# Optimization experiments

Hardware: AMD Instinct MI355X
Metric: run time of the kernel (lower is better)

The kernel has to match this reference:

```python
import jax, jax.numpy as jnp
import numpy as np
from jax import lax

BS, T, GRID, FEAT = 64, 32, 36, 256
HID, PROJ, NCLS = 256, 128, 6
MLP_IN = FEAT + HID  # 512


def _lstm(h, c, xs, Wih, Whh, bih, bhh):
    # xs: (L, bs, in); PyTorch gate order i, f, g, o
    def step(carry, x):
        h, c = carry
        g = x @ Wih.T + bih + h @ Whh.T + bhh
        i_, f_, g_, o_ = jnp.split(g, 4, axis=-1)
        c = jax.nn.sigmoid(f_) * c + jax.nn.sigmoid(i_) * jnp.tanh(g_)
        h = jax.nn.sigmoid(o_) * jnp.tanh(c)
        return (h, c), None
    (h, c), _ = lax.scan(step, (h, c), xs)
    return h, c


def setup_inputs() -> dict:
    key = jax.random.key(0)
    ks = iter(jax.random.split(key, 32))
    r = lambda *s: jax.random.normal(next(ks), s, dtype=jnp.float32) * 0.05
    inp = {
        'cnn_feat_seq': jax.random.normal(next(ks), (BS, T, GRID, FEAT), dtype=jnp.float32),
        'gaze_seq': jax.random.normal(next(ks), (BS, T, 3), dtype=jnp.float32),
        # spatial attention layer
        'W_lh': r(PROJ, HID), 'b_lh': r(PROJ),      # linear_lstm
        'W_cn': r(PROJ, FEAT), 'b_cn': r(PROJ),     # linear_cnn
        'w_wt': r(1, PROJ),                         # linear_weight (no bias)
        # gaze LSTM
        'Wih': r(4 * HID, 3), 'Whh': r(4 * HID, HID), 'bih': r(4 * HID), 'bhh': r(4 * HID),
        # init hidden / cell MLPs (Linear, Tanh, Linear, Tanh)
        'Wh1': r(HID, 3), 'bh1': r(HID), 'Wh2': r(HID, HID), 'bh2': r(HID),
        'Wc1': r(HID, 3), 'bc1': r(HID), 'Wc2': r(HID, HID), 'bc2': r(HID),
        # mlp classifier (3 linears, no activations)
        'Wm1': r(MLP_IN, MLP_IN), 'bm1': r(MLP_IN),
        'Wm2': r(MLP_IN, MLP_IN), 'bm2': r(MLP_IN),
        'Wm3': r(NCLS, MLP_IN), 'bm3': r(NCLS),
    }
    return inp


def reference(cnn_feat_seq, gaze_seq, W_lh, b_lh, W_cn, b_cn, w_wt,
              Wih, Whh, bih, bhh, Wh1, bh1, Wh2, bh2, Wc1, bc1, Wc2, bc2,
              Wm1, bm1, Wm2, bm2, Wm3, bm3):
    bs, num_frame, grid, feat = cnn_feat_seq.shape
    # init LSTM state: Sequential(Linear,Tanh,Linear,Tanh) then an extra F.tanh
    mg = jnp.mean(gaze_seq, axis=1)  # (bs, 3)
    h = jnp.tanh(jnp.tanh(jnp.tanh(mg @ Wh1.T + bh1) @ Wh2.T + bh2))
    c = jnp.tanh(jnp.tanh(jnp.tanh(mg @ Wc1.T + bc1) @ Wc2.T + bc2))

    preds = []
    for i in range(num_frame):
        V = cnn_feat_seq[:, i]  # (bs, grid, feat)
        # attention scores; same Linear applied per grid cell -> compute once
        Hl = h @ W_lh.T + b_lh                       # (bs, proj)
        Vp = V @ W_cn.T + b_cn                       # (bs, grid, proj)
        z = jnp.tanh(Hl[:, None, :] + Vp) @ w_wt[0]  # (bs, grid)
        # replicate torch.cat(dim=0).view(bs, grid): flat order is grid-major
        z_scrambled = z.T.reshape(bs, grid)
        sw = jax.nn.softmax(z_scrambled, axis=1)     # (bs, grid)
        spatial_feat = jnp.einsum('bgf,bg->bf', V, sw)
        # LSTM over growing gaze prefix (frame 0: first step only)
        L = 1 if i == 0 else i
        xs = jnp.transpose(gaze_seq[:, :L, :], (1, 0, 2))  # (L, bs, 3)
        h, c = _lstm(h, c, xs, Wih, Whh, bih, bhh)
        fc = jnp.concatenate([spatial_feat, h], axis=1)    # (bs, 512)
        pred = ((fc @ Wm1.T + bm1) @ Wm2.T + bm2) @ Wm3.T + bm3
        preds.append(pred[None])  # (1, bs, ncls)
    # torch.cat(pred_all, 1) over (1,bs,ncls) pieces -> (1, T*bs, ncls)
    return jnp.concatenate(preds, axis=1)
```

## Files before the change

### kernel.cpp

```cpp
#include <hip/hip_runtime.h>
#include <math.h>


typedef _Float16 h2_t __attribute__((ext_vector_type(2)));

#if __has_builtin(__builtin_amdgcn_fdot2)
#define HAVE_FDOT2 1
#else
#define HAVE_FDOT2 0
#endif

__device__ __forceinline__ float dot2(unsigned w, unsigned h, float acc) {
#if HAVE_FDOT2
  return __builtin_amdgcn_fdot2(__builtin_bit_cast(h2_t, w),
                                __builtin_bit_cast(h2_t, h), acc, false);
#else
  h2_t a = __builtin_bit_cast(h2_t, w);
  h2_t b = __builtin_bit_cast(h2_t, h);
  return acc + (float)a[0] * (float)b[0] + (float)a[1] * (float)b[1];
#endif
}

__device__ __forceinline__ unsigned pack2(float a, float b) {
  h2_t p;
  p[0] = (_Float16)a;
  p[1] = (_Float16)b;
  return __builtin_bit_cast(unsigned, p);
}

__device__ __forceinline__ float sigmoid_f(float x) {
  return __builtin_amdgcn_rcpf(1.f + __expf(-x));
}
__device__ __forceinline__ float tanh_f(float x) {
  return 1.f - 2.f * __builtin_amdgcn_rcpf(1.f + __expf(2.f * x));
}

__global__ void k_pack_lstm(const float* __restrict__ Whh,
                            unsigned* __restrict__ wlds_pack,
                            unsigned* __restrict__ wst) {
  const int idx = blockIdx.x * 256 + threadIdx.x;
  if (idx < 32768) {
    const int row = idx >> 5, pair = idx & 31;
    wlds_pack[idx] =
        pack2(Whh[row * 256 + 2 * pair], Whh[row * 256 + 2 * pair + 1]);
  } else {
    const int rel = idx - 32768;
    const int m = rel >> 12, row = (rel >> 2) & 1023, d = rel & 3;
    const int pair = 32 + 4 * m + d;
    wst[rel] = pack2(Whh[row * 256 + 2 * pair], Whh[row * 256 + 2 * pair + 1]);
  }
}

__global__ void k_packh2(const float* __restrict__ src,
                         unsigned* __restrict__ dst, int n) {
  const int i = blockIdx.x * 256 + threadIdx.x;
  if (i < n) dst[i] = pack2(src[2 * i], src[2 * i + 1]);
}

__global__ void k_xg(const float* __restrict__ gaze,
                     const float* __restrict__ Wih,
                     const float* __restrict__ bih,
                     const float* __restrict__ bhh,
                     float* __restrict__ xg) {
  const int idx = blockIdx.x * 256 + threadIdx.x;
  if (idx >= 31 * 64 * 1024) return;
  const int j = idx & 1023;
  const int b = (idx >> 10) & 63;
  const int t = idx >> 16;
  const float* gz = gaze + (b * 32 + t) * 3;
  xg[idx] = gz[0] * Wih[j * 3 + 0] + gz[1] * Wih[j * 3 + 1] +
            gz[2] * Wih[j * 3 + 2] + bih[j] + bhh[j];
}

__global__ void k_init(const float* __restrict__ gaze,
                       const float* __restrict__ Wh1, const float* __restrict__ bh1,
                       const float* __restrict__ Wh2, const float* __restrict__ bh2,
                       const float* __restrict__ Wc1, const float* __restrict__ bc1,
                       const float* __restrict__ Wc2, const float* __restrict__ bc2,
                       float* __restrict__ HH, float* __restrict__ c0) {
  const int b = blockIdx.x;
  const int tid = threadIdx.x;
  __shared__ float mg[3];
  __shared__ float t1h[256], t1c[256];
  if (tid < 3) {
    float s = 0.f;
    for (int t = 0; t < 32; t++) s += gaze[(b * 32 + t) * 3 + tid];
    mg[tid] = s * (1.f / 32.f);
  }
  __syncthreads();
  {
    float a = mg[0] * Wh1[tid * 3 + 0] + mg[1] * Wh1[tid * 3 + 1] +
              mg[2] * Wh1[tid * 3 + 2] + bh1[tid];
    t1h[tid] = tanhf(a);
    float c = mg[0] * Wc1[tid * 3 + 0] + mg[1] * Wc1[tid * 3 + 1] +
              mg[2] * Wc1[tid * 3 + 2] + bc1[tid];
    t1c[tid] = tanhf(c);
  }
  __syncthreads();
  float s1 = bh2[tid], s2 = bc2[tid];
  for (int k = 0; k < 256; k++) {
    s1 += t1h[k] * Wh2[tid * 256 + k];
    s2 += t1c[k] * Wc2[tid * 256 + k];
  }
  HH[b * 256 + tid] = tanhf(tanhf(s1));
  c0[b * 256 + tid] = tanhf(tanhf(s2));
}

__global__ __launch_bounds__(1024) void k_fused(
    const float* __restrict__ xg, const unsigned* __restrict__ wst,
    const unsigned* __restrict__ wlds_pack, const float* __restrict__ c0,
    float* __restrict__ HH, const float* __restrict__ cnn,
    const unsigned* __restrict__ wcn_h2, const float* __restrict__ bcn,
    unsigned* __restrict__ Vp, int nvp, const float* __restrict__ Wm1,
    unsigned* __restrict__ wm1d, const float* __restrict__ Wm2,
    unsigned* __restrict__ wm2d, const float* __restrict__ Wm3,
    unsigned* __restrict__ wm3d, const float* __restrict__ Wlh,
    unsigned* __restrict__ wlhd) {
  const int bid = blockIdx.x;
  const int tid = threadIdx.x;
  __shared__ __align__(16) unsigned smem[38016];

  if (bid < 64) {
    const int b = bid;
    unsigned* wlds = smem;
    float* actl = (float*)(smem + 36864);
    unsigned* h2l = smem + 36864 + 1024;

    for (int i = tid; i < 1024 * 32; i += 1024) {
      const int row = i >> 5, p = i & 31;
      wlds[row * 36 + p] = wlds_pack[i];
    }

    float cst = (tid < 256) ? c0[b * 256 + tid] : 0.f;
    if (tid < 256) ((_Float16*)h2l)[tid] = (_Float16)HH[b * 256 + tid];
    __syncthreads();

    const unsigned* wA = &wlds[tid * 36];
    const uint4* wstp = (const uint4*)wst + tid;
    const bool is_g = (tid >= 512) & (tid < 768);
    float hval = 0.f;

    for (int frame = 0; frame < 32; frame++) {
      const int L = frame ? frame : 1;
      for (int t = 0; t < L; t++) {
        const float xgv = xg[(t * 64 + b) * 1024 + tid];
        float ga0 = 0.f, ga1 = 0.f;
#pragma unroll
        for (int q = 0; q < 8; q++) {
          const uint4 h4 = *(const uint4*)&h2l[4 * q];
          const uint4 a4 = *(const uint4*)&wA[4 * q];
          if ((q & 1) == 0) {
            ga0 = dot2(a4.x, h4.x, ga0);
            ga0 = dot2(a4.y, h4.y, ga0);
            ga0 = dot2(a4.z, h4.z, ga0);
            ga0 = dot2(a4.w, h4.w, ga0);
          } else {
            ga1 = dot2(a4.x, h4.x, ga1);
            ga1 = dot2(a4.y, h4.y, ga1);
            ga1 = dot2(a4.z, h4.z, ga1);
            ga1 = dot2(a4.w, h4.w, ga1);
          }
        }
#pragma unroll
        for (int m = 0; m < 24; m++) {
          const uint4 wq = wstp[m << 10];
          const uint4 h4 = *(const uint4*)&h2l[32 + 4 * m];
          if ((m & 1) == 0) {
            ga0 = dot2(wq.x, h4.x, ga0);
            ga0 = dot2(wq.y, h4.y, ga0);
            ga0 = dot2(wq.z, h4.z, ga0);
            ga0 = dot2(wq.w, h4.w, ga0);
          } else {
            ga1 = dot2(wq.x, h4.x, ga1);
            ga1 = dot2(wq.y, h4.y, ga1);
            ga1 = dot2(wq.z, h4.z, ga1);
            ga1 = dot2(wq.w, h4.w, ga1);
          }
        }
        const float g = ga0 + ga1 + xgv;
        const float act = is_g ? tanh_f(g) : sigmoid_f(g);
        actl[tid] = act;
        __syncthreads();
        if (tid < 256) {
          const float i_ = actl[tid];
          const float f_ = actl[256 + tid];
          const float g_ = actl[512 + tid];
          const float o_ = actl[768 + tid];
          cst = f_ * cst + i_ * g_;
          hval = o_ * tanh_f(cst);
          ((_Float16*)h2l)[tid] = (_Float16)hval;
        }
        __syncthreads();
      }
      if (tid < 256) HH[((frame + 1) * 64 + b) * 256 + tid] = hval;
    }
  } else if (bid < 64 + nvp) {
    const int vb = bid - 64;
    const int i = vb / 18, rt = vb - 18 * i;
    const int r0 = rt * 128;
    unsigned* As = smem;
    unsigned* Bs = smem + 16896;
    float* bcs = (float*)(smem + 33792);

    for (int idx = tid; idx < 128 * 128; idx += 1024) {
      const int r = idx >> 7, kp = idx & 127;
      const int R = r0 + r;
      const int b = R / 36, g = R - b * 36;
      const float* src = cnn + (((size_t)b * 32 + i) * 36 + g) * 256 + 2 * kp;
      As[r * 132 + kp] = pack2(src[0], src[1]);
    }
    for (int idx = tid; idx < 128 * 128; idx += 1024) {
      const int o = idx >> 7, kp = idx & 127;
      Bs[o * 132 + kp] = wcn_h2[o * 128 + kp];
    }
    if (tid < 128) bcs[tid] = bcn[tid];
    __syncthreads();

    const int ry = tid >> 4, px = tid & 15;
    float acc[2][8];
#pragma unroll
    for (int k = 0; k < 2; k++)
#pragma unroll
      for (int m = 0; m < 8; m++)
        acc[k][m] = bcs[32 * (m >> 1) + 2 * px + (m & 1)];
    for (int kb = 0; kb < 32; kb++) {
      uint4 a4[2], b4[8];
#pragma unroll
      for (int k = 0; k < 2; k++)
        a4[k] = *(const uint4*)&As[(64 * k + ry) * 132 + 4 * kb];
#pragma unroll
      for (int m = 0; m < 8; m++)
        b4[m] = *(const uint4*)&Bs[(32 * (m >> 1) + 2 * px + (m & 1)) * 132 + 4 * kb];
#pragma unroll
      for (int k = 0; k < 2; k++)
#pragma unroll
        for (int m = 0; m < 8; m++) {
          acc[k][m] = dot2(a4[k].x, b4[m].x, acc[k][m]);
          acc[k][m] = dot2(a4[k].y, b4[m].y, acc[k][m]);
          acc[k][m] = dot2(a4[k].z, b4[m].z, acc[k][m]);
          acc[k][m] = dot2(a4[k].w, b4[m].w, acc[k][m]);
        }
    }
#pragma unroll
    for (int k = 0; k < 2; k++) {
      const int R = r0 + 64 * k + ry;
#pragma unroll
      for (int jj = 0; jj < 4; jj++)
        Vp[((size_t)i * 2304 + R) * 64 + 16 * jj + px] =
            pack2(acc[k][2 * jj], acc[k][2 * jj + 1]);
    }
  } else {
    const int pb = bid - 64 - nvp;
    if (pb < 8) {
      const int base = pb * 16384;
      for (int j = tid; j < 16384; j += 1024)
        wm1d[base + j] = pack2(Wm1[2 * (base + j)], Wm1[2 * (base + j) + 1]);
    } else if (pb < 16) {
      const int base = (pb - 8) * 16384;
      for (int j = tid; j < 16384; j += 1024)
        wm2d[base + j] = pack2(Wm2[2 * (base + j)], Wm2[2 * (base + j) + 1]);
    } else {
      for (int j = tid; j < 1536; j += 1024)
        wm3d[j] = pack2(Wm3[2 * j], Wm3[2 * j + 1]);
      for (int j = tid; j < 16384; j += 1024)
        wlhd[j] = pack2(Wlh[2 * j], Wlh[2 * j + 1]);
    }
  }
}

__global__ void k_zfin(const unsigned* __restrict__ Vp,
                       const float* __restrict__ Hl,
                       const float* __restrict__ wwt,
                       float* __restrict__ zbuf) {
  const int bid = blockIdx.x;
  const int i = bid / 18, rt = bid - 18 * i;
  const int r0 = rt * 128;
  const int tid = threadIdx.x;
  __shared__ float Hls[5 * 128];
  __shared__ float wws[128];
  __shared__ float zpart[128 * 16];
  const int bmin = r0 / 36;
  for (int idx = tid; idx < 5 * 128; idx += 256) {
    const int bb = bmin + (idx >> 7);
    if (bb < 64) Hls[idx] = Hl[(i * 64 + bb) * 128 + (idx & 127)];
  }
  if (tid < 128) wws[tid] = wwt[tid];
  __syncthreads();
  const int ry = tid >> 4, px = tid & 15;
#pragma unroll
  for (int k = 0; k < 8; k++) {
    const int r = 16 * k + ry;
    const int R = r0 + r;
    const int b = R / 36;
    const unsigned* vr = Vp + ((size_t)i * 2304 + R) * 64;
    const float* Hr = &Hls[(b - bmin) * 128];
    float z = 0.f;
#pragma unroll
    for (int jj = 0; jj < 4; jj++) {
      const int pp = 16 * jj + px;
      const h2_t pr = __builtin_bit_cast(h2_t, vr[pp]);
      z += wws[2 * pp] * tanh_f(Hr[2 * pp] + (float)pr[0]);
      z += wws[2 * pp + 1] * tanh_f(Hr[2 * pp + 1] + (float)pr[1]);
    }
    zpart[r * 16 + px] = z;
  }
  __syncthreads();
  if (tid < 128) {
    float z = 0.f;
#pragma unroll
    for (int x = 0; x < 16; x++) z += zpart[tid * 16 + x];
    const int R = r0 + tid;
    const int b = R / 36, g = R - b * 36;
    zbuf[(i * 64 + b) * 36 + g] = z;
  }
}

__global__ void k_hl(const float* __restrict__ HH,
                     const unsigned* __restrict__ wlh_h2,
                     const float* __restrict__ blh, float* __restrict__ Hl) {
  const int i = blockIdx.x;
  const int tid = threadIdx.x;
  __shared__ __align__(16) unsigned Ah[64 * 132];
  __shared__ __align__(16) unsigned Bh[128 * 132];
  for (int idx = tid; idx < 64 * 128; idx += 256) {
    const int r = idx >> 7, kp = idx & 127;
    const float* s = HH + ((size_t)(i * 64 + r)) * 256 + 2 * kp;
    Ah[r * 132 + kp] = pack2(s[0], s[1]);
  }
  for (int idx = tid; idx < 128 * 128; idx += 256) {
    const int o = idx >> 7, kp = idx & 127;
    Bh[o * 132 + kp] = wlh_h2[o * 128 + kp];
  }
  __syncthreads();
  const int ry = tid >> 4, px = tid & 15;
  float acc[4][8];
#pragma unroll
  for (int k = 0; k < 4; k++)
#pragma unroll
    for (int j = 0; j < 8; j++) acc[k][j] = 0.f;
  for (int kb = 0; kb < 32; kb++) {
    uint4 a4[4], b4[8];
#pragma unroll
    for (int k = 0; k < 4; k++) a4[k] = *(const uint4*)&Ah[(16 * k + ry) * 132 + 4 * kb];
#pragma unroll
    for (int j = 0; j < 8; j++) b4[j] = *(const uint4*)&Bh[(16 * j + px) * 132 + 4 * kb];
#pragma unroll
    for (int k = 0; k < 4; k++)
#pragma unroll
      for (int j = 0; j < 8; j++) {
        acc[k][j] = dot2(a4[k].x, b4[j].x, acc[k][j]);
        acc[k][j] = dot2(a4[k].y, b4[j].y, acc[k][j]);
        acc[k][j] = dot2(a4[k].z, b4[j].z, acc[k][j]);
        acc[k][j] = dot2(a4[k].w, b4[j].w, acc[k][j]);
      }
  }
#pragma unroll
  for (int k = 0; k < 4; k++)
#pragma unroll
    for (int j = 0; j < 8; j++)
      Hl[(i * 64 + 16 * k + ry) * 128 + 16 * j + px] = acc[k][j] + blh[16 * j + px];
}

__global__ void k_att_z(const float* __restrict__ cnn,
                        const unsigned* __restrict__ wcn_h2,
                        const float* __restrict__ bcn,
                        const float* __restrict__ Hl,
                        const float* __restrict__ wwt,
                        float* __restrict__ zbuf) {
  const int bid = blockIdx.x;
  const int i = bid / 18, rt = bid - 18 * i;
  const int tid = threadIdx.x;
  const int r0 = rt * 128;
  __shared__ __align__(16) unsigned As[128 * 132];
  __shared__ __align__(16) unsigned Bs[128 * 132];
  __shared__ float zpart[128 * 16];
  __shared__ float Hls[5 * 128];
  __shared__ float wws[128];
  __shared__ float bcs[128];

  for (int idx = tid; idx < 128 * 128; idx += 256) {
    const int r = idx >> 7, kp = idx & 127;
    const int R = r0 + r;
    const int b = R / 36, g = R - b * 36;
    const float* src = cnn + (((size_t)b * 32 + i) * 36 + g) * 256 + 2 * kp;
    As[r * 132 + kp] = pack2(src[0], src[1]);
  }
  for (int idx = tid; idx < 128 * 128; idx += 256) {
    const int o = idx >> 7, kp = idx & 127;
    Bs[o * 132 + kp] = wcn_h2[o * 128 + kp];
  }
  const int bmin = r0 / 36;
  for (int idx = tid; idx < 5 * 128; idx += 256) {
    const int bb = bmin + (idx >> 7);
    if (bb < 64) Hls[idx] = Hl[(i * 64 + bb) * 128 + (idx & 127)];
  }
  if (tid < 128) {
    wws[tid] = wwt[tid];
    bcs[tid] = bcn[tid];
  }
  __syncthreads();

  const int ry = tid >> 4, px = tid & 15;
  float acc[8][8];
#pragma unroll
  for (int k = 0; k < 8; k++)
#pragma unroll
    for (int j = 0; j < 8; j++) acc[k][j] = bcs[16 * j + px];
  for (int kb = 0; kb < 32; kb++) {
    uint4 a4[8], b4[8];
#pragma unroll
    for (int k = 0; k < 8; k++) a4[k] = *(const uint4*)&As[(16 * k + ry) * 132 + 4 * kb];
#pragma unroll
    for (int j = 0; j < 8; j++) b4[j] = *(const uint4*)&Bs[(16 * j + px) * 132 + 4 * kb];
#pragma unroll
    for (int k = 0; k < 8; k++)
#pragma unroll
      for (int j = 0; j < 8; j++) {
        acc[k][j] = dot2(a4[k].x, b4[j].x, acc[k][j]);
        acc[k][j] = dot2(a4[k].y, b4[j].y, acc[k][j]);
        acc[k][j] = dot2(a4[k].z, b4[j].z, acc[k][j]);
        acc[k][j] = dot2(a4[k].w, b4[j].w, acc[k][j]);
      }
  }
#pragma unroll
  for (int k = 0; k < 8; k++) {
    const int r = 16 * k + ry;
    const int R = r0 + r;
    const int b = R / 36;
    const float* HlRow = &Hls[(b - bmin) * 128];
    float zp = 0.f;
#pragma unroll
    for (int j = 0; j < 8; j++) {
      const int po = 16 * j + px;
      zp += wws[po] * tanh_f(HlRow[po] + acc[k][j]);
    }
    zpart[r * 16 + px] = zp;
  }
  __syncthreads();
  if (tid < 128) {
    float z = 0.f;
#pragma unroll
    for (int x = 0; x < 16; x++) z += zpart[tid * 16 + x];
    const int R = r0 + tid;
    const int b = R / 36, g = R - b * 36;
    zbuf[(i * 64 + b) * 36 + g] = z;
  }
}

__global__ void k_att_sf(const float* __restrict__ cnn,
                         const float* __restrict__ zbuf,
                         const float* __restrict__ HH,
                         float* __restrict__ fc) {
  const int bid = blockIdx.x;
  const int i = bid >> 6, b = bid & 63;
  const int tid = threadIdx.x;
  __shared__ float zl[36];
  __shared__ float el[40];
  __shared__ float red[1];
  if (tid < 36) {
    const int idx = b * 36 + tid;
    zl[tid] = zbuf[(i * 64 + (idx & 63)) * 36 + (idx >> 6)];
  }
  __syncthreads();
  if (tid == 0) {
    float m = zl[0];
    for (int g = 1; g < 36; g++) m = fmaxf(m, zl[g]);
    float s = 0.f;
    for (int g = 0; g < 36; g++) {
      const float e = __expf(zl[g] - m);
      el[g] = e;
      s += e;
    }
    red[0] = 1.f / s;
  }
  __syncthreads();
  const float inv = red[0];
  float accv = 0.f;
  const float* Vb = cnn + (((size_t)b * 32 + i) * 36) * 256 + tid;
#pragma unroll 4
  for (int g = 0; g < 36; g++) accv += el[g] * Vb[g * 256];
  fc[(size_t)bid * 512 + tid] = accv * inv;
  fc[(size_t)bid * 512 + 256 + tid] = HH[((i + 1) * 64 + b) * 256 + tid];
}

template <int SRCMODE>
__global__ void k_mlp(const void* __restrict__ src,
                      const unsigned* __restrict__ wh2,
                      const float* __restrict__ bias,
                      unsigned* __restrict__ dst) {
  const int bid = blockIdx.x;
  const int nb = bid >> 2, ob = bid & 3;
  const int n0 = nb * 64, o0 = ob * 128;
  const int tid = threadIdx.x;
  __shared__ __align__(16) unsigned As[64 * 132];
  __shared__ __align__(16) unsigned Bs[128 * 132];
  const int ry = tid >> 4, px = tid & 15;
  float acc[4][8];
#pragma unroll
  for (int k = 0; k < 4; k++)
#pragma unroll
    for (int m = 0; m < 8; m++)
      acc[k][m] = bias[o0 + 32 * (m >> 1) + 2 * px + (m & 1)];
  for (int kc = 0; kc < 2; kc++) {
    __syncthreads();
    for (int idx = tid; idx < 64 * 128; idx += 256) {
      const int r = idx >> 7, kp = idx & 127;
      if (SRCMODE == 0) {
        const float* s = (const float*)src + ((size_t)(n0 + r)) * 512 + kc * 256 + 2 * kp;
        As[r * 132 + kp] = pack2(s[0], s[1]);
      } else {
        As[r * 132 + kp] = ((const unsigned*)src)[((size_t)(n0 + r)) * 256 + kc * 128 + kp];
      }
    }
    for (int idx = tid; idx < 128 * 128; idx += 256) {
      const int o = idx >> 7, kp = idx & 127;
      Bs[o * 132 + kp] = wh2[((size_t)(o0 + o)) * 256 + kc * 128 + kp];
    }
    __syncthreads();
    for (int kb = 0; kb < 32; kb++) {
      uint4 a4[4], b4[8];
#pragma unroll
      for (int k = 0; k < 4; k++)
        a4[k] = *(const uint4*)&As[(16 * k + ry) * 132 + 4 * kb];
#pragma unroll
      for (int m = 0; m < 8; m++)
        b4[m] = *(const uint4*)&Bs[(32 * (m >> 1) + 2 * px + (m & 1)) * 132 + 4 * kb];
#pragma unroll
      for (int k = 0; k < 4; k++)
#pragma unroll
        for (int m = 0; m < 8; m++) {
          acc[k][m] = dot2(a4[k].x, b4[m].x, acc[k][m]);
          acc[k][m] = dot2(a4[k].y, b4[m].y, acc[k][m]);
          acc[k][m] = dot2(a4[k].z, b4[m].z, acc[k][m]);
          acc[k][m] = dot2(a4[k].w, b4[m].w, acc[k][m]);
        }
    }
  }
#pragma unroll
  for (int k = 0; k < 4; k++) {
    const int n = n0 + 16 * k + ry;
#pragma unroll
    for (int j = 0; j < 4; j++)
      dst[(size_t)n * 256 + (o0 >> 1) + 16 * j + px] =
          pack2(acc[k][2 * j], acc[k][2 * j + 1]);
  }
}

__global__ void k_mlp3(const unsigned* __restrict__ y2h2,
                       const unsigned* __restrict__ wm3h2,
                       const float* __restrict__ bm3,
                       float* __restrict__ out) {
  const int nb = blockIdx.x;
  const int tid = threadIdx.x;
  __shared__ __align__(16) unsigned Ys[64 * 256];
  __shared__ __align__(16) unsigned Ws[6 * 256];
  for (int idx = tid; idx < 64 * 256; idx += 256)
    Ys[idx] = y2h2[(size_t)nb * 64 * 256 + idx];
  for (int idx = tid; idx < 6 * 256; idx += 256) Ws[idx] = wm3h2[idx];
  __syncthreads();
  for (int u = 0; u < 2; u++) {
    const int idx = tid + u * 256;
    if (idx < 384) {
      const int nl = idx / 6, c = idx - 6 * nl;
      float a0 = 0.f, a1 = 0.f;
#pragma unroll
      for (int kq = 0; kq < 64; kq++) {
        const uint4 y4 = *(const uint4*)&Ys[nl * 256 + 4 * kq];
        const uint4 w4 = *(const uint4*)&Ws[c * 256 + 4 * kq];
        a0 = dot2(y4.x, w4.x, a0);
        a1 = dot2(y4.y, w4.y, a1);
        a0 = dot2(y4.z, w4.z, a0);
        a1 = dot2(y4.w, w4.w, a1);
      }
      out[(size_t)(nb * 64 + nl) * 6 + c] = a0 + a1 + bm3[c];
    }
  }
}

extern "C" void kernel_launch(void* const* d_in, const int* in_sizes, int n_in,
                              void* d_out, int out_size, void* d_ws,
                              size_t ws_size, hipStream_t stream) {
  (void)in_sizes; (void)n_in; (void)out_size;
  const float* cnn  = (const float*)d_in[0];
  const float* gaze = (const float*)d_in[1];
  const float* W_lh = (const float*)d_in[2];
  const float* b_lh = (const float*)d_in[3];
  const float* W_cn = (const float*)d_in[4];
  const float* b_cn = (const float*)d_in[5];
  const float* w_wt = (const float*)d_in[6];
  const float* Wih  = (const float*)d_in[7];
  const float* Whh  = (const float*)d_in[8];
  const float* bih  = (const float*)d_in[9];
  const float* bhh  = (const float*)d_in[10];
  const float* Wh1  = (const float*)d_in[11];
  const float* bh1  = (const float*)d_in[12];
  const float* Wh2  = (const float*)d_in[13];
  const float* bh2  = (const float*)d_in[14];
  const float* Wc1  = (const float*)d_in[15];
  const float* bc1  = (const float*)d_in[16];
  const float* Wc2  = (const float*)d_in[17];
  const float* bc2  = (const float*)d_in[18];
  const float* Wm1  = (const float*)d_in[19];
  const float* bm1  = (const float*)d_in[20];
  const float* Wm2  = (const float*)d_in[21];
  const float* bm2  = (const float*)d_in[22];
  const float* Wm3  = (const float*)d_in[23];
  const float* bm3  = (const float*)d_in[24];
  float* out = (float*)d_out;

  unsigned* W = (unsigned*)d_ws;
  float* Wf = (float*)d_ws;
  const size_t O_xg  = 0;
  const size_t O_wl  = 2031616;
  const size_t O_wst = O_wl + 32768;
  const size_t O_HH  = O_wst + 98304;
  const size_t O_c0  = O_HH + 540672;
  const size_t O_Hl  = O_c0 + 16384;
  const size_t O_z   = O_Hl + 262144;
  const size_t O_fc  = O_z + 73728;
  const size_t O_y1  = O_fc + 1048576;
  const size_t O_y2  = O_y1 + 524288;
  const size_t O_wcn = O_y2 + 524288;
  const size_t O_wlh = O_wcn + 16384;
  const size_t O_wm1 = O_wlh + 16384;
  const size_t O_wm2 = O_wm1 + 131072;
  const size_t O_wm3 = O_wm2 + 131072;
  const size_t O_vp  = O_wm3 + 1536;
  const size_t needed = (O_vp + 4718592) * 4ull;

  const bool big = ws_size >= needed;
  const int nvp = big ? 576 : 0;

  float* xg  = Wf + O_xg;
  float* HH  = Wf + O_HH;
  float* c0f = Wf + O_c0;
  float* Hlf = Wf + O_Hl;
  float* zf  = Wf + O_z;
  float* fcf = Wf + O_fc;
  unsigned* Vp = W + O_vp;

  k_pack_lstm<<<512, 256, 0, stream>>>(Whh, W + O_wl, W + O_wst);
  k_packh2<<<64, 256, 0, stream>>>(W_cn, W + O_wcn, 16384);
  k_xg<<<7936, 256, 0, stream>>>(gaze, Wih, bih, bhh, xg);
  k_init<<<64, 256, 0, stream>>>(gaze, Wh1, bh1, Wh2, bh2, Wc1, bc1, Wc2, bc2,
                                 HH, c0f);
  k_fused<<<64 + nvp + 17, 1024, 0, stream>>>(
      xg, W + O_wst, W + O_wl, c0f, HH, cnn, W + O_wcn, b_cn, Vp, nvp, Wm1,
      W + O_wm1, Wm2, W + O_wm2, Wm3, W + O_wm3, W_lh, W + O_wlh);
  k_hl<<<32, 256, 0, stream>>>(HH, W + O_wlh, b_lh, Hlf);
  if (big)
    k_zfin<<<576, 256, 0, stream>>>(Vp, Hlf, w_wt, zf);
  else
    k_att_z<<<576, 256, 0, stream>>>(cnn, W + O_wcn, b_cn, Hlf, w_wt, zf);
  k_att_sf<<<2048, 256, 0, stream>>>(cnn, zf, HH, fcf);
  k_mlp<0><<<128, 256, 0, stream>>>((const void*)fcf, W + O_wm1, bm1, W + O_y1);
  k_mlp<1><<<128, 256, 0, stream>>>((const void*)(W + O_y1), W + O_wm2, bm2, W + O_y2);
  k_mlp3<<<32, 256, 0, stream>>>(W + O_y2, W + O_wm3, bm3, out);
}
```

Before: 1.073 ms.

## Stream LSTM recurrent weights as e5m2 bytes and merge prep kernels

The part of the recurrent Whh weights streamed from global memory each LSTM step is now stored as 8-bit e5m2, made by rounding fp16 to its high byte. It is expanded back to fp16 pairs with byte permutes before the dot2 products, which halves the bytes read per step on the serial LSTM critical path. Separately, the four preprocessing kernels (weight packing, W_cn packing, input-gate precompute, init state MLP) are merged into one launch to save launch overhead. The cost is extra permute instructions and a loss of mantissa precision in most recurrent weights, which may push the result past the accuracy tolerance.

```diff
diff --git a/kernel.cpp b/kernel.cpp
--- a/kernel.cpp
+++ b/kernel.cpp
@@ -8,6 +8,12 @@
 #define HAVE_FDOT2 1
 #else
 #define HAVE_FDOT2 0
+#endif
+
+#if __has_builtin(__builtin_amdgcn_perm)
+#define USE_E5M2 1
+#else
+#define USE_E5M2 0
 #endif
 
 __device__ __forceinline__ float dot2(unsigned w, unsigned h, float acc) {
@@ -35,75 +41,102 @@
   return 1.f - 2.f * __builtin_amdgcn_rcpf(1.f + __expf(2.f * x));
 }
 
-__global__ void k_pack_lstm(const float* __restrict__ Whh,
-                            unsigned* __restrict__ wlds_pack,
-                            unsigned* __restrict__ wst) {
-  const int idx = blockIdx.x * 256 + threadIdx.x;
-  if (idx < 32768) {
-    const int row = idx >> 5, pair = idx & 31;
-    wlds_pack[idx] =
-        pack2(Whh[row * 256 + 2 * pair], Whh[row * 256 + 2 * pair + 1]);
+__device__ __forceinline__ unsigned enc_e5m2_4(float a, float b, float c,
+                                               float d) {
+  unsigned r = 0;
+  unsigned short h;
+  h = __builtin_bit_cast(unsigned short, (_Float16)a);
+  r |= (((unsigned)h + 0x80u) >> 8) & 0xFFu;
+  h = __builtin_bit_cast(unsigned short, (_Float16)b);
+  r |= ((((unsigned)h + 0x80u) >> 8) & 0xFFu) << 8;
+  h = __builtin_bit_cast(unsigned short, (_Float16)c);
+  r |= ((((unsigned)h + 0x80u) >> 8) & 0xFFu) << 16;
+  h = __builtin_bit_cast(unsigned short, (_Float16)d);
+  r |= ((((unsigned)h + 0x80u) >> 8) & 0xFFu) << 24;
+  return r;
+}
+
+#if USE_E5M2
+#define STREAM_DW 49152
+#else
+#define STREAM_DW 98304
+#endif
+#define PACK_DW (32768 + STREAM_DW)
+#define NPACK (PACK_DW / 256)
+
+__global__ __launch_bounds__(256) void k_pre(
+    const float* __restrict__ Whh, unsigned* __restrict__ wlds_pack,
+    unsigned* __restrict__ wst, const float* __restrict__ W_cn,
+    unsigned* __restrict__ wcn_h2, const float* __restrict__ gaze,
+    const float* __restrict__ Wih, const float* __restrict__ bih,
+    const float* __restrict__ bhh, float* __restrict__ xg,
+    const float* __restrict__ Wh1, const float* __restrict__ bh1,
+    const float* __restrict__ Wh2, const float* __restrict__ bh2,
+    const float* __restrict__ Wc1, const float* __restrict__ bc1,
+    const float* __restrict__ Wc2, const float* __restrict__ bc2,
+    float* __restrict__ HH, float* __restrict__ c0) {
+  const int bid = blockIdx.x;
+  const int tid = threadIdx.x;
+  if (bid < NPACK) {
+    const int idx = bid * 256 + tid;
+    if (idx < 32768) {
+      const int row = idx >> 5, pair = idx & 31;
+      wlds_pack[idx] =
+          pack2(Whh[row * 256 + 2 * pair], Whh[row * 256 + 2 * pair + 1]);
+    } else {
+#if USE_E5M2
+      const int rel = idx - 32768;
+      const int m = rel >> 12, row = (rel >> 2) & 1023, d = rel & 3;
+      const float* wr = Whh + row * 256 + 64 + 16 * m + 4 * d;
+      wst[rel] = enc_e5m2_4(wr[0], wr[1], wr[2], wr[3]);
+#else
+      const int rel = idx - 32768;
+      const int m = rel >> 12, row = (rel >> 2) & 1023, d = rel & 3;
+      const int pair = 32 + 4 * m + d;
+      wst[rel] =
+          pack2(Whh[row * 256 + 2 * pair], Whh[row * 256 + 2 * pair + 1]);
+#endif
+    }
+  } else if (bid < NPACK + 64) {
+    const int i = (bid - NPACK) * 256 + tid;
+    wcn_h2[i] = pack2(W_cn[2 * i], W_cn[2 * i + 1]);
+  } else if (bid < NPACK + 64 + 7936) {
+    const int idx = (bid - NPACK - 64) * 256 + tid;
+    if (idx < 31 * 64 * 1024) {
+      const int j = idx & 1023;
+      const int b = (idx >> 10) & 63;
+      const int t = idx >> 16;
+      const float* gz = gaze + (b * 32 + t) * 3;
+      xg[idx] = gz[0] * Wih[j * 3 + 0] + gz[1] * Wih[j * 3 + 1] +
+                gz[2] * Wih[j * 3 + 2] + bih[j] + bhh[j];
+    }
   } else {
-    const int rel = idx - 32768;
-    const int m = rel >> 12, row = (rel >> 2) & 1023, d = rel & 3;
-    const int pair = 32 + 4 * m + d;
-    wst[rel] = pack2(Whh[row * 256 + 2 * pair], Whh[row * 256 + 2 * pair + 1]);
-  }
-}
-
-__global__ void k_packh2(const float* __restrict__ src,
-                         unsigned* __restrict__ dst, int n) {
-  const int i = blockIdx.x * 256 + threadIdx.x;
-  if (i < n) dst[i] = pack2(src[2 * i], src[2 * i + 1]);
-}
-
-__global__ void k_xg(const float* __restrict__ gaze,
-                     const float* __restrict__ Wih,
-                     const float* __restrict__ bih,
-                     const float* __restrict__ bhh,
-                     float* __restrict__ xg) {
-  const int idx = blockIdx.x * 256 + threadIdx.x;
-  if (idx >= 31 * 64 * 1024) return;
-  const int j = idx & 1023;
-  const int b = (idx >> 10) & 63;
-  const int t = idx >> 16;
-  const float* gz = gaze + (b * 32 + t) * 3;
-  xg[idx] = gz[0] * Wih[j * 3 + 0] + gz[1] * Wih[j * 3 + 1] +
-            gz[2] * Wih[j * 3 + 2] + bih[j] + bhh[j];
-}
-
-__global__ void k_init(const float* __restrict__ gaze,
-                       const float* __restrict__ Wh1, const float* __restrict__ bh1,
-                       const float* __restrict__ Wh2, const float* __restrict__ bh2,
-                       const float* __restrict__ Wc1, const float* __restrict__ bc1,
-                       const float* __restrict__ Wc2, const float* __restrict__ bc2,
-                       float* __restrict__ HH, float* __restrict__ c0) {
-  const int b = blockIdx.x;
-  const int tid = threadIdx.x;
-  __shared__ float mg[3];
-  __shared__ float t1h[256], t1c[256];
-  if (tid < 3) {
-    float s = 0.f;
-    for (int t = 0; t < 32; t++) s += gaze[(b * 32 + t) * 3 + tid];
-    mg[tid] = s * (1.f / 32.f);
-  }
-  __syncthreads();
-  {
-    float a = mg[0] * Wh1[tid * 3 + 0] + mg[1] * Wh1[tid * 3 + 1] +
-              mg[2] * Wh1[tid * 3 + 2] + bh1[tid];
-    t1h[tid] = tanhf(a);
-    float c = mg[0] * Wc1[tid * 3 + 0] + mg[1] * Wc1[tid * 3 + 1] +
-              mg[2] * Wc1[tid * 3 + 2] + bc1[tid];
-    t1c[tid] = tanhf(c);
-  }
-  __syncthreads();
-  float s1 = bh2[tid], s2 = bc2[tid];
-  for (int k = 0; k < 256; k++) {
-    s1 += t1h[k] * Wh2[tid * 256 + k];
-    s2 += t1c[k] * Wc2[tid * 256 + k];
-  }
-  HH[b * 256 + tid] = tanhf(tanhf(s1));
-  c0[b * 256 + tid] = tanhf(tanhf(s2));
+    const int b = bid - NPACK - 64 - 7936;
+    __shared__ float mg[3];
+    __shared__ float t1h[256], t1c[256];
+    if (tid < 3) {
+      float s = 0.f;
+      for (int t = 0; t < 32; t++) s += gaze[(b * 32 + t) * 3 + tid];
+      mg[tid] = s * (1.f / 32.f);
+    }
+    __syncthreads();
+    {
+      float a = mg[0] * Wh1[tid * 3 + 0] + mg[1] * Wh1[tid * 3 + 1] +
+                mg[2] * Wh1[tid * 3 + 2] + bh1[tid];
+      t1h[tid] = tanhf(a);
+      float c = mg[0] * Wc1[tid * 3 + 0] + mg[1] * Wc1[tid * 3 + 1] +
+                mg[2] * Wc1[tid * 3 + 2] + bc1[tid];
+      t1c[tid] = tanhf(c);
+    }
+    __syncthreads();
+    float s1 = bh2[tid], s2 = bc2[tid];
+    for (int k = 0; k < 256; k++) {
+      s1 += t1h[k] * Wh2[tid * 256 + k];
+      s2 += t1c[k] * Wc2[tid * 256 + k];
+    }
+    HH[b * 256 + tid] = tanhf(tanhf(s1));
+    c0[b * 256 + tid] = tanhf(tanhf(s2));
+  }
 }
 
 __global__ __launch_bounds__(1024) void k_fused(
@@ -161,6 +194,22 @@
             ga1 = dot2(a4.w, h4.w, ga1);
           }
         }
+#if USE_E5M2
+#pragma unroll
+        for (int m = 0; m < 12; m++) {
+          const uint4 wq = wstp[m << 10];
+          const uint4 ha = *(const uint4*)&h2l[32 + 8 * m];
+          const uint4 hb = *(const uint4*)&h2l[36 + 8 * m];
+          ga0 = dot2(__builtin_amdgcn_perm(wq.x, 0u, 0x050C040Cu), ha.x, ga0);
+          ga0 = dot2(__builtin_amdgcn_perm(wq.x, 0u, 0x070C060Cu), ha.y, ga0);
+          ga1 = dot2(__builtin_amdgcn_perm(wq.y, 0u, 0x050C040Cu), ha.z, ga1);
+          ga1 = dot2(__builtin_amdgcn_perm(wq.y, 0u, 0x070C060Cu), ha.w, ga1);
+          ga0 = dot2(__builtin_amdgcn_perm(wq.z, 0u, 0x050C040Cu), hb.x, ga0);
+          ga0 = dot2(__builtin_amdgcn_perm(wq.z, 0u, 0x070C060Cu), hb.y, ga0);
+          ga1 = dot2(__builtin_amdgcn_perm(wq.w, 0u, 0x050C040Cu), hb.z, ga1);
+          ga1 = dot2(__builtin_amdgcn_perm(wq.w, 0u, 0x070C060Cu), hb.w, ga1);
+        }
+#else
 #pragma unroll
         for (int m = 0; m < 24; m++) {
           const uint4 wq = wstp[m << 10];
@@ -177,6 +226,7 @@
             ga1 = dot2(wq.w, h4.w, ga1);
           }
         }
+#endif
         const float g = ga0 + ga1 + xgv;
         const float act = is_g ? tanh_f(g) : sigmoid_f(g);
         actl[tid] = act;
@@ -639,11 +689,9 @@
   float* fcf = Wf + O_fc;
   unsigned* Vp = W + O_vp;
 
-  k_pack_lstm<<<512, 256, 0, stream>>>(Whh, W + O_wl, W + O_wst);
-  k_packh2<<<64, 256, 0, stream>>>(W_cn, W + O_wcn, 16384);
-  k_xg<<<7936, 256, 0, stream>>>(gaze, Wih, bih, bhh, xg);
-  k_init<<<64, 256, 0, stream>>>(gaze, Wh1, bh1, Wh2, bh2, Wc1, bc1, Wc2, bc2,
-                                 HH, c0f);
+  k_pre<<<NPACK + 64 + 7936 + 64, 256, 0, stream>>>(
+      Whh, W + O_wl, W + O_wst, W_cn, W + O_wcn, gaze, Wih, bih, bhh, xg, Wh1,
+      bh1, Wh2, bh2, Wc1, bc1, Wc2, bc2, HH, c0f);
   k_fused<<<64 + nvp + 17, 1024, 0, stream>>>(
       xg, W + O_wst, W + O_wl, c0f, HH, cnn, W + O_wcn, b_cn, Vp, nvp, Wm1,
       W + O_wm1, Wm2, W + O_wm2, Wm3, W + O_wm3, W_lh, W + O_wlh);
```

After: 1.153 ms. 7.5% more time.
